# Performance work log

Hardware: AMD Instinct MI355X
Metric: run time of the kernel (lower is better)

## Reference

```python
import jax, jax.numpy as jnp
import numpy as np

K = 16
SIGMA_ONE = 0.02
EXP_RANGE = 10.0
T_MIN = 1e-6


def setup_inputs() -> dict:
    key = jax.random.key(0)
    ks = jax.random.split(key, 6)
    B, D, H = 32, 49152, 16
    return {
        "mu": jax.random.normal(ks[0], (B, D), dtype=jnp.float32),
        "t": jax.random.uniform(ks[1], (B, 1), dtype=jnp.float32),
        "W1": jax.random.normal(ks[2], (2, H), dtype=jnp.float32) * 0.5,
        "b1": jax.random.normal(ks[3], (H,), dtype=jnp.float32) * 0.1,
        "W2": jax.random.normal(ks[4], (H, 2), dtype=jnp.float32) * 0.1,
        "b2": jax.random.normal(ks[5], (2,), dtype=jnp.float32) * 0.1,
    }


def reference(mu, t, W1, b1, W2, b2):
    # bin geometry: centers (2K-1)/K - 1 for K=1..k, lower/upper = center -/+ 1/k
    k_idx = jnp.arange(1, K + 1, dtype=mu.dtype)
    k_centers = (2.0 * k_idx - 1.0) / K - 1.0          # [K]
    k_lower = k_centers - 1.0 / K
    k_upper = k_centers + 1.0 / K

    gamma = 1.0 - jnp.power(jnp.asarray(SIGMA_ONE, mu.dtype), 2.0 * t)  # [B,1]

    # inner model: pointwise MLP on stacked (mu, t) -> (mean_eps, log_var_eps)
    x = jnp.stack([mu, jnp.broadcast_to(t, mu.shape)], axis=-1)  # [B,D,2]
    h = jax.nn.gelu(x @ W1 + b1)                                 # [B,D,H]
    out = h @ W2 + b2                                            # [B,D,2]
    mu_eps, ln_sigma_eps = out[..., 0], out[..., 1]

    var_scale = jnp.sqrt((1.0 - gamma) / gamma)                  # [B,1]
    mu_x = mu / gamma - var_scale * mu_eps                       # [B,D]
    sigma_x = jnp.maximum(
        var_scale * jnp.exp(jnp.clip(ln_sigma_eps, -EXP_RANGE, EXP_RANGE)),
        SIGMA_ONE,
    )
    cond = t < T_MIN                                             # [B,1]
    mu_x = jnp.where(cond, 0.0, mu_x)
    sigma_x = jnp.where(cond, 1.0, sigma_x)

    inv = (1.0 / (sigma_x * jnp.sqrt(jnp.asarray(2.0, mu.dtype))))[..., None]  # [B,D,1]
    mu_b = mu_x[..., None]                                       # [B,D,1]

    def normal_cdf(bins):  # bins [K] -> [B,D,K]
        return 0.5 * (1.0 + jax.lax.erf((bins - mu_b) * inv))

    cdf_lower = jnp.where(k_lower <= -1.0, 0.0, normal_cdf(k_lower))
    cdf_upper = jnp.where(k_upper >= 1.0, 1.0, normal_cdf(k_upper))
    return cdf_upper - cdf_lower                                 # [B,D,K]
```

## Files before the change

### kernel.cpp

```cpp
#include <hip/hip_runtime.h>
#include <math.h>

#define KBINS 16
#define HID 16
#define LN_SIGMA1 (-3.912023005428146f)

__device__ __forceinline__ float to_sgpr(float x) {
    return __int_as_float(__builtin_amdgcn_readfirstlane(__float_as_int(x)));
}

__global__ __launch_bounds__(256, 4) void bfn_kernel(
    const float* __restrict__ mu,
    const float* __restrict__ t,
    const float* __restrict__ W1,
    const float* __restrict__ b1,
    const float* __restrict__ W2,
    const float* __restrict__ b2,
    float* __restrict__ out,
    int D)
{
    __shared__ float lds[256 * 20];

    const int b   = blockIdx.y;
    const int tid = threadIdx.x;
    const int d0  = blockIdx.x * 256;
    const int d   = d0 + tid;
    const bool valid = (d < D);

    const float tb    = t[b];
    const float gamma = -expm1f(2.0f * tb * LN_SIGMA1);
    const float e2t   = 1.0f - gamma;
    const float inv_gamma = 1.0f / gamma;
    const float var_scale = sqrtf(e2t * inv_gamma);
    const bool  tiny_t = (tb < 1e-6f);

    float w1a[HID], c1[HID], w20[HID], w21[HID];
#pragma unroll
    for (int i = 0; i < HID; ++i) {
        w1a[i] = to_sgpr(W1[i]);
        c1[i]  = fmaf(tb, W1[HID + i], b1[i]);
        w20[i] = to_sgpr(W2[2 * i]);
        w21[i] = to_sgpr(W2[2 * i + 1]);
    }
    const float bias0 = to_sgpr(b2[0]);
    const float bias1 = to_sgpr(b2[1]);

    const float m = valid ? mu[(size_t)b * D + d] : 0.0f;

    float o0 = bias0, o1 = bias1;
#pragma unroll
    for (int i = 0; i < HID; ++i) {
        float pre = fmaf(m, w1a[i], c1[i]);
        float p2  = pre * pre;
        float z   = pre * fmaf(p2, -0.0713552235f, -1.5957691216f);
        float e   = __expf(z);
        float h   = pre * __builtin_amdgcn_rcpf(1.0f + e);
        o0 = fmaf(h, w20[i], o0);
        o1 = fmaf(h, w21[i], o1);
    }

    float mu_x = fmaf(m, inv_gamma, -var_scale * o0);
    float lse  = fminf(fmaxf(o1, -10.0f), 10.0f);
    float sigma_x = fmaxf(var_scale * __expf(lse), 0.02f);
    if (tiny_t) { mu_x = 0.0f; sigma_x = 1.0f; }

    const float inv = 0.70710678118f * __builtin_amdgcn_rcpf(sigma_x);
    const float x0  = (-0.875f - mu_x) * inv;
    const float stp = 0.125f * inv;

    float cdf[KBINS + 1];
    cdf[0] = 0.0f; cdf[KBINS] = 1.0f;
#pragma unroll
    for (int j = 1; j < KBINS; ++j) {
        float x  = fmaf((float)(j - 1), stp, x0);
        float ax = fabsf(x);
        float p  = fmaf(0.078108f, ax, 0.000972f);
        p        = fmaf(p, ax, 0.230389f);
        p        = fmaf(p, ax, 0.278393f);
        float q  = fmaf(p, ax, 1.0f);
        float q2 = q * q;
        float q4 = q2 * q2;
        float hr = 0.5f * __builtin_amdgcn_rcpf(q4);
        cdf[j] = (x >= 0.0f) ? (1.0f - hr) : hr;
    }

    const bool full = (d0 + 256 <= D);
    if (full) {
        float4* row = (float4*)(lds + tid * 20);
#pragma unroll
        for (int s = 0; s < 4; ++s)
            row[s] = make_float4(cdf[4*s+1] - cdf[4*s],   cdf[4*s+2] - cdf[4*s+1],
                                 cdf[4*s+3] - cdf[4*s+2], cdf[4*s+4] - cdf[4*s+3]);
        __syncthreads();
        float4* og = (float4*)out + ((size_t)b * D + d0) * 4;
#pragma unroll
        for (int s = 0; s < 4; ++s) {
            int f = s * 256 + tid;
            int e = f >> 2;
            int c = (f & 3) << 2;
            og[f] = *(const float4*)(lds + e * 20 + c);
        }
    } else if (valid) {
        float4* op = (float4*)(out + ((size_t)b * D + d) * (size_t)KBINS);
#pragma unroll
        for (int s = 0; s < 4; ++s)
            op[s] = make_float4(cdf[4*s+1] - cdf[4*s],   cdf[4*s+2] - cdf[4*s+1],
                                 cdf[4*s+3] - cdf[4*s+2], cdf[4*s+4] - cdf[4*s+3]);
    }
}

extern "C" void kernel_launch(void* const* d_in, const int* in_sizes, int n_in,
                              void* d_out, int out_size, void* d_ws, size_t ws_size,
                              hipStream_t stream) {
    const float* mu = (const float*)d_in[0];
    const float* t  = (const float*)d_in[1];
    const float* W1 = (const float*)d_in[2];
    const float* b1 = (const float*)d_in[3];
    const float* W2 = (const float*)d_in[4];
    const float* b2 = (const float*)d_in[5];
    float* out = (float*)d_out;

    const int B = in_sizes[1];
    const int D = in_sizes[0] / B;

    dim3 block(256);
    dim3 grid((D + 255) / 256, B);
    bfn_kernel<<<grid, block, 0, stream>>>(mu, t, W1, b1, W2, b2, out, D);
}
```

Measured before the change: 125.8 us.

## Replace LDS transpose with wave shuffles, compute CDFs per output quad, nontemporal stores

Drops the shared-memory staging and block barrier used to coalesce the output. Each lane now fetches the per-element offset and step of a neighbouring element with __shfl and computes the CDF values for one 4-bin quad, then writes that float4 directly with a nontemporal store. Adjacent lanes therefore write contiguous 16-byte chunks. Each thread now evaluates 20 CDF approximations (some shared boundaries are recomputed) instead of 15, and it issues shuffles in place of LDS traffic. The launch bounds occupancy hint rises from 4 to 6 to match the lower LDS and register pressure.

Result: no change. 127.3 us (+1.2%).

```diff
diff --git a/kernel.cpp b/kernel.cpp
--- a/kernel.cpp
+++ b/kernel.cpp
@@ -5,11 +5,24 @@
 #define HID 16
 #define LN_SIGMA1 (-3.912023005428146f)
 
+typedef __attribute__((ext_vector_type(4))) float f32x4;
+
 __device__ __forceinline__ float to_sgpr(float x) {
     return __int_as_float(__builtin_amdgcn_readfirstlane(__float_as_int(x)));
 }
 
-__global__ __launch_bounds__(256, 4) void bfn_kernel(
+__device__ __forceinline__ float phi_fast(float x) {
+    float ax = fabsf(x);
+    float p  = fmaf(0.078108f, ax, 0.000972f);
+    p        = fmaf(p, ax, 0.230389f);
+    p        = fmaf(p, ax, 0.278393f);
+    float q  = fmaf(p, ax, 1.0f);
+    float q2 = q * q;
+    float hr = 0.5f * __builtin_amdgcn_rcpf(q2 * q2);
+    return (x >= 0.0f) ? (1.0f - hr) : hr;
+}
+
+__global__ __launch_bounds__(256, 6) void bfn_kernel(
     const float* __restrict__ mu,
     const float* __restrict__ t,
     const float* __restrict__ W1,
@@ -19,19 +32,16 @@
     float* __restrict__ out,
     int D)
 {
-    __shared__ float lds[256 * 20];
-
-    const int b   = blockIdx.y;
-    const int tid = threadIdx.x;
-    const int d0  = blockIdx.x * 256;
-    const int d   = d0 + tid;
-    const bool valid = (d < D);
+    const int b    = blockIdx.y;
+    const int tid  = threadIdx.x;
+    const int lane = tid & 63;
+    const int d0   = blockIdx.x * 256;
+    const int d    = d0 + tid;
 
     const float tb    = t[b];
     const float gamma = -expm1f(2.0f * tb * LN_SIGMA1);
-    const float e2t   = 1.0f - gamma;
     const float inv_gamma = 1.0f / gamma;
-    const float var_scale = sqrtf(e2t * inv_gamma);
+    const float var_scale = sqrtf((1.0f - gamma) * inv_gamma);
     const bool  tiny_t = (tb < 1e-6f);
 
     float w1a[HID], c1[HID], w20[HID], w21[HID];
@@ -42,19 +52,18 @@
         w20[i] = to_sgpr(W2[2 * i]);
         w21[i] = to_sgpr(W2[2 * i + 1]);
     }
-    const float bias0 = to_sgpr(b2[0]);
-    const float bias1 = to_sgpr(b2[1]);
 
-    const float m = valid ? mu[(size_t)b * D + d] : 0.0f;
+    const bool full = (d0 + 256 <= D);
+    const float m = (full || d < D) ? mu[(size_t)b * D + d] : 0.0f;
 
-    float o0 = bias0, o1 = bias1;
+    float o0 = to_sgpr(b2[0]);
+    float o1 = to_sgpr(b2[1]);
 #pragma unroll
     for (int i = 0; i < HID; ++i) {
         float pre = fmaf(m, w1a[i], c1[i]);
         float p2  = pre * pre;
         float z   = pre * fmaf(p2, -0.0713552235f, -1.5957691216f);
-        float e   = __expf(z);
-        float h   = pre * __builtin_amdgcn_rcpf(1.0f + e);
+        float h   = pre * __builtin_amdgcn_rcpf(1.0f + __expf(z));
         o0 = fmaf(h, w20[i], o0);
         o1 = fmaf(h, w21[i], o1);
     }
@@ -65,42 +74,33 @@
     if (tiny_t) { mu_x = 0.0f; sigma_x = 1.0f; }
 
     const float inv = 0.70710678118f * __builtin_amdgcn_rcpf(sigma_x);
-    const float x0  = (-0.875f - mu_x) * inv;
-    const float stp = 0.125f * inv;
+    const float xb = (-1.0f - mu_x) * inv;
+    const float st = 0.125f * inv;
 
-    float cdf[KBINS + 1];
-    cdf[0] = 0.0f; cdf[KBINS] = 1.0f;
-#pragma unroll
-    for (int j = 1; j < KBINS; ++j) {
-        float x  = fmaf((float)(j - 1), stp, x0);
-        float ax = fabsf(x);
-        float p  = fmaf(0.078108f, ax, 0.000972f);
-        p        = fmaf(p, ax, 0.230389f);
-        p        = fmaf(p, ax, 0.278393f);
-        float q  = fmaf(p, ax, 1.0f);
-        float q2 = q * q;
-        float q4 = q2 * q2;
-        float hr = 0.5f * __builtin_amdgcn_rcpf(q4);
-        cdf[j] = (x >= 0.0f) ? (1.0f - hr) : hr;
-    }
-
-    const bool full = (d0 + 256 <= D);
     if (full) {
-        float4* row = (float4*)(lds + tid * 20);
-#pragma unroll
-        for (int s = 0; s < 4; ++s)
-            row[s] = make_float4(cdf[4*s+1] - cdf[4*s],   cdf[4*s+2] - cdf[4*s+1],
-                                 cdf[4*s+3] - cdf[4*s+2], cdf[4*s+4] - cdf[4*s+3]);
-        __syncthreads();
-        float4* og = (float4*)out + ((size_t)b * D + d0) * 4;
+        const int   q   = lane & 3;
+        const float fj0 = (float)(q * 4);
+        const size_t ebase = (size_t)b * D + d0 + (tid & ~63);
 #pragma unroll
         for (int s = 0; s < 4; ++s) {
-            int f = s * 256 + tid;
-            int e = f >> 2;
-            int c = (f & 3) << 2;
-            og[f] = *(const float4*)(lds + e * 20 + c);
+            int   el  = s * 16 + (lane >> 2);
+            float xbe = __shfl(xb, el, 64);
+            float ste = __shfl(st, el, 64);
+            float c0 = (q == 0) ? 0.0f : phi_fast(fmaf(fj0,        ste, xbe));
+            float c1v =                  phi_fast(fmaf(fj0 + 1.0f, ste, xbe));
+            float c2 =                   phi_fast(fmaf(fj0 + 2.0f, ste, xbe));
+            float c3 =                   phi_fast(fmaf(fj0 + 3.0f, ste, xbe));
+            float c4 = (q == 3) ? 1.0f : phi_fast(fmaf(fj0 + 4.0f, ste, xbe));
+            f32x4 r;
+            r.x = c1v - c0; r.y = c2 - c1v; r.z = c3 - c2; r.w = c4 - c3;
+            __builtin_nontemporal_store(r, (f32x4*)out + (ebase + el) * 4 + q);
         }
-    } else if (valid) {
+    } else if (d < D) {
+        float cdf[KBINS + 1];
+        cdf[0] = 0.0f; cdf[KBINS] = 1.0f;
+#pragma unroll
+        for (int j = 1; j < KBINS; ++j)
+            cdf[j] = phi_fast(fmaf((float)j, st, xb));
         float4* op = (float4*)(out + ((size_t)b * D + d) * (size_t)KBINS);
 #pragma unroll
         for (int s = 0; s < 4; ++s)
```
